# Optimization experiments

Hardware: AMD Instinct MI355X
Metric: run time of the kernel (lower is better)

## Reference

```python
import jax, jax.numpy as jnp
import numpy as np

N = 50000
E = 800000
IN_DIM = 256
HID = 64
HEADS = 4
OUT_DIM = 32
NEG_SLOPE = 0.2
EPS = 1e-5


def segment_softmax(logits, seg, num_segments):
    # logits: [E, H]; softmax over edges sharing the same destination node
    m = jax.ops.segment_max(logits, seg, num_segments=num_segments)
    m = jnp.where(jnp.isfinite(m), m, 0.0)
    e = jnp.exp(logits - m[seg])
    s = jax.ops.segment_sum(e, seg, num_segments=num_segments)
    return e / (s[seg] + 1e-16)


def setup_inputs() -> dict:
    key = jax.random.key(0)
    ks = jax.random.split(key, 16)
    d = {}
    d['x'] = jax.random.normal(ks[0], (N, IN_DIM), dtype=jnp.float32)
    d['edge_index'] = jax.random.randint(ks[1], (2, E), 0, N, dtype=jnp.int64)
    sc = lambda fan: 1.0 / np.sqrt(fan)
    # input transform: Linear(256->128), Linear(128->64)
    d['t1_w'] = jax.random.normal(ks[2], (IN_DIM, IN_DIM // 2), dtype=jnp.float32) * sc(IN_DIM)
    d['t1_b'] = jnp.zeros((IN_DIM // 2,), jnp.float32)
    d['t2_w'] = jax.random.normal(ks[3], (IN_DIM // 2, IN_DIM // 4), dtype=jnp.float32) * sc(IN_DIM // 2)
    d['t2_b'] = jnp.zeros((IN_DIM // 4,), jnp.float32)
    d['g1_w'] = jax.random.normal(ks[4], (IN_DIM // 4, HEADS * HID), dtype=jnp.float32) * sc(IN_DIM // 4)
    d['g1_att_src'] = jax.random.normal(ks[5], (HEADS, HID), dtype=jnp.float32) * sc(HID)
    d['g1_att_dst'] = jax.random.normal(ks[6], (HEADS, HID), dtype=jnp.float32) * sc(HID)
    d['g1_b'] = jnp.zeros((HEADS * HID,), jnp.float32)
    # GraphNorm(256)
    d['gn_w'] = jnp.ones((HEADS * HID,), jnp.float32)
    d['gn_b'] = jnp.zeros((HEADS * HID,), jnp.float32)
    d['gn_ms'] = jnp.ones((HEADS * HID,), jnp.float32)
    # GATConv 2: 256 -> 32, 1 head, no concat (mean == identity for 1 head)
    d['g2_w'] = jax.random.normal(ks[7], (HEADS * HID, OUT_DIM), dtype=jnp.float32) * sc(HEADS * HID)
    d['g2_att_src'] = jax.random.normal(ks[8], (1, OUT_DIM), dtype=jnp.float32) * sc(OUT_DIM)
    d['g2_att_dst'] = jax.random.normal(ks[9], (1, OUT_DIM), dtype=jnp.float32) * sc(OUT_DIM)
    d['g2_b'] = jnp.zeros((OUT_DIM,), jnp.float32)
    return d


def gat_conv(x, src, dst, w, att_src, att_dst, bias, n_nodes):
    heads, ch = att_src.shape
    h = (x @ w).reshape(n_nodes, heads, ch)            # [N,H,C]
    a_src = jnp.sum(h * att_src, axis=-1)              # [N,H]
    a_dst = jnp.sum(h * att_dst, axis=-1)              # [N,H]
    logits = jax.nn.leaky_relu(a_src[src] + a_dst[dst], NEG_SLOPE)  # [E,H]
    alpha = segment_softmax(logits, dst, n_nodes)      # [E,H]
    msgs = alpha[:, :, None] * h[src]                  # [E,H,C]
    out = jax.ops.segment_sum(msgs, dst, num_segments=n_nodes)  # [N,H,C]
    return out.reshape(n_nodes, heads * ch) + bias


def reference(x, edge_index, t1_w, t1_b, t2_w, t2_b,
              g1_w, g1_att_src, g1_att_dst, g1_b,
              gn_w, gn_b, gn_ms,
              g2_w, g2_att_src, g2_att_dst, g2_b):
    src, dst = edge_index[0], edge_index[1]
    # input transform (dropout inactive in eval)
    h = jax.nn.relu(x @ t1_w + t1_b)
    h = jax.nn.relu(h @ t2_w + t2_b)
    # GAT layer 1 (concat heads)
    h = gat_conv(h, src, dst, g1_w, g1_att_src, g1_att_dst, g1_b, N)
    # GraphNorm over the whole graph (batch=None -> single graph)
    mean = jnp.mean(h, axis=0)
    o = h - mean * gn_ms
    var = jnp.mean(o * o, axis=0)
    h = o / jnp.sqrt(var + EPS) * gn_w + gn_b
    h = jax.nn.elu(h)
    # GAT layer 2 (1 head, concat=False)
    h = gat_conv(h, src, dst, g2_w, g2_att_src, g2_att_dst, g2_b, N)
    return jax.nn.log_softmax(h, axis=1)
```

## Files before the change

### kernel.cpp

```cpp
#include <hip/hip_runtime.h>

#define NSLOPE 0.2f
#define GEPS 1e-5f

typedef unsigned short ushortT;
typedef __attribute__((ext_vector_type(8))) unsigned short us8;
typedef __attribute__((ext_vector_type(8))) __bf16 bf16x8;
typedef __attribute__((ext_vector_type(4))) float f32x4;

__device__ __forceinline__ float lrelu(float x) { return x >= 0.f ? x : NSLOPE * x; }
__device__ __forceinline__ ushortT f2bf(float f) {
    unsigned int u = __float_as_uint(f);
    return (ushortT)((u + 0x7fffu + ((u >> 16) & 1u)) >> 16);
}
__device__ __forceinline__ float bf2f(ushortT h) {
    return __uint_as_float((unsigned int)h << 16);
}

__global__ __launch_bounds__(256) void k_prep(
    const float* __restrict__ w1, const float* __restrict__ w2,
    const float* __restrict__ g1w, const float* __restrict__ g2w,
    ushortT* __restrict__ w1t, ushortT* __restrict__ w2t,
    ushortT* __restrict__ g1t, ushortT* __restrict__ g2t)
{
    const int i = blockIdx.x * 256 + threadIdx.x;
    if (i < 128 * 256) { const int c = i >> 8, k = i & 255; w1t[i] = f2bf(w1[k * 128 + c]); }
    if (i < 64 * 128)  { const int c = i >> 7, k = i & 127; w2t[i] = f2bf(w2[k * 64 + c]); }
    if (i < 256 * 64)  { const int c = i >> 6, k = i & 63;  g1t[i] = f2bf(g1w[k * 256 + c]); }
    if (i < 32 * 256)  { const int c = i >> 8, k = i & 255; g2t[i] = f2bf(g2w[k * 32 + c]); }
}

__global__ __launch_bounds__(256) void k_lin1(const float* __restrict__ x,
    const ushortT* __restrict__ w1t, const float* __restrict__ b1,
    ushortT* __restrict__ h1, int n)
{
    __shared__ us8 Ab[64 * 128 / 16];
    __shared__ us8 Bb[128 * 128 / 16];
    char* A = (char*)Ab; char* B = (char*)Bb;
    const int t = threadIdx.x;
    const int w = t >> 6, l = t & 63;
    const int lo = l & 15, hi = l >> 4;
    const int n0 = blockIdx.x * 64;
    const int wm = (w >> 1) * 32, wn = (w & 1) * 64;
    f32x4 acc[2][4];
    #pragma unroll
    for (int mf = 0; mf < 2; ++mf)
        #pragma unroll
        for (int nf = 0; nf < 4; ++nf) acc[mf][nf] = (f32x4){0.f, 0.f, 0.f, 0.f};

    const int arow = t >> 2, ak0 = (t & 3) * 16;
    int agn = n0 + arow; if (agn >= n) agn = n - 1;
    const int asw = (arow & 7) << 4;

    for (int kc = 0; kc < 4; ++kc) {
        __syncthreads();
        {
            ushortT tmp[16];
            const float* xp = &x[(size_t)agn * 256 + kc * 64 + ak0];
            #pragma unroll
            for (int j = 0; j < 4; ++j) {
                const float4 v = *(const float4*)(xp + j * 4);
                tmp[j*4+0] = f2bf(v.x); tmp[j*4+1] = f2bf(v.y);
                tmp[j*4+2] = f2bf(v.z); tmp[j*4+3] = f2bf(v.w);
            }
            *(us8*)(A + arow * 128 + ((ak0 * 2) ^ asw)) = *(us8*)tmp;
            *(us8*)(A + arow * 128 + ((ak0 * 2 + 16) ^ asw)) = *(us8*)(tmp + 8);
        }
        #pragma unroll
        for (int i = 0; i < 4; ++i) {
            const int idx = i * 256 + t, br = idx >> 3, bs = idx & 7;
            const us8 v = *(const us8*)&w1t[(size_t)br * 256 + kc * 64 + bs * 8];
            *(us8*)(B + br * 128 + ((bs * 16) ^ ((br & 7) << 4))) = v;
        }
        __syncthreads();
        #pragma unroll
        for (int ks = 0; ks < 2; ++ks) {
            const int koff = ks * 64 + hi * 16;
            bf16x8 af[2], bf[4];
            #pragma unroll
            for (int mf = 0; mf < 2; ++mf) {
                const int r = wm + mf * 16 + lo;
                af[mf] = *(const bf16x8*)(A + r * 128 + (koff ^ ((r & 7) << 4)));
            }
            #pragma unroll
            for (int nf = 0; nf < 4; ++nf) {
                const int r = wn + nf * 16 + lo;
                bf[nf] = *(const bf16x8*)(B + r * 128 + (koff ^ ((r & 7) << 4)));
            }
            #pragma unroll
            for (int mf = 0; mf < 2; ++mf)
                #pragma unroll
                for (int nf = 0; nf < 4; ++nf)
                    acc[mf][nf] = __builtin_amdgcn_mfma_f32_16x16x32_bf16(af[mf], bf[nf], acc[mf][nf], 0, 0, 0);
        }
    }
    #pragma unroll
    for (int nf = 0; nf < 4; ++nf) {
        const int col = wn + nf * 16 + lo;
        const float bb = b1[col];
        #pragma unroll
        for (int mf = 0; mf < 2; ++mf)
            #pragma unroll
            for (int j = 0; j < 4; ++j) {
                const int r = n0 + wm + mf * 16 + hi * 4 + j;
                if (r < n) h1[(size_t)r * 128 + col] = f2bf(fmaxf(acc[mf][nf][j] + bb, 0.f));
            }
    }
}

__global__ __launch_bounds__(256) void k_lin2(const ushortT* __restrict__ h1,
    const ushortT* __restrict__ w2t, const float* __restrict__ b2,
    ushortT* __restrict__ h2, int n)
{
    __shared__ us8 Ab[64 * 128 / 16];
    __shared__ us8 Bb[64 * 128 / 16];
    char* A = (char*)Ab; char* B = (char*)Bb;
    const int t = threadIdx.x;
    const int w = t >> 6, l = t & 63;
    const int lo = l & 15, hi = l >> 4;
    const int n0 = blockIdx.x * 64;
    const int wm = (w >> 1) * 32, wn = (w & 1) * 32;
    f32x4 acc[2][2];
    #pragma unroll
    for (int mf = 0; mf < 2; ++mf)
        #pragma unroll
        for (int nf = 0; nf < 2; ++nf) acc[mf][nf] = (f32x4){0.f, 0.f, 0.f, 0.f};

    const int arow = t >> 2, ak0 = (t & 3) * 16;
    int agn = n0 + arow; if (agn >= n) agn = n - 1;
    const int asw = (arow & 7) << 4;

    for (int kc = 0; kc < 2; ++kc) {
        __syncthreads();
        {
            const us8 v0 = *(const us8*)&h1[(size_t)agn * 128 + kc * 64 + ak0];
            const us8 v1 = *(const us8*)&h1[(size_t)agn * 128 + kc * 64 + ak0 + 8];
            *(us8*)(A + arow * 128 + ((ak0 * 2) ^ asw)) = v0;
            *(us8*)(A + arow * 128 + ((ak0 * 2 + 16) ^ asw)) = v1;
        }
        #pragma unroll
        for (int i = 0; i < 2; ++i) {
            const int idx = i * 256 + t, br = idx >> 3, bs = idx & 7;
            const us8 v = *(const us8*)&w2t[(size_t)br * 128 + kc * 64 + bs * 8];
            *(us8*)(B + br * 128 + ((bs * 16) ^ ((br & 7) << 4))) = v;
        }
        __syncthreads();
        #pragma unroll
        for (int ks = 0; ks < 2; ++ks) {
            const int koff = ks * 64 + hi * 16;
            bf16x8 af[2], bf[2];
            #pragma unroll
            for (int mf = 0; mf < 2; ++mf) {
                const int r = wm + mf * 16 + lo;
                af[mf] = *(const bf16x8*)(A + r * 128 + (koff ^ ((r & 7) << 4)));
            }
            #pragma unroll
            for (int nf = 0; nf < 2; ++nf) {
                const int r = wn + nf * 16 + lo;
                bf[nf] = *(const bf16x8*)(B + r * 128 + (koff ^ ((r & 7) << 4)));
            }
            #pragma unroll
            for (int mf = 0; mf < 2; ++mf)
                #pragma unroll
                for (int nf = 0; nf < 2; ++nf)
                    acc[mf][nf] = __builtin_amdgcn_mfma_f32_16x16x32_bf16(af[mf], bf[nf], acc[mf][nf], 0, 0, 0);
        }
    }
    #pragma unroll
    for (int nf = 0; nf < 2; ++nf) {
        const int col = wn + nf * 16 + lo;
        const float bb = b2[col];
        #pragma unroll
        for (int mf = 0; mf < 2; ++mf)
            #pragma unroll
            for (int j = 0; j < 4; ++j) {
                const int r = n0 + wm + mf * 16 + hi * 4 + j;
                if (r < n) h2[(size_t)r * 64 + col] = f2bf(fmaxf(acc[mf][nf][j] + bb, 0.f));
            }
    }
}

__global__ __launch_bounds__(256) void k_g1feat(const ushortT* __restrict__ h2,
    const ushortT* __restrict__ g1t, const float* __restrict__ attS, const float* __restrict__ attD,
    ushortT* __restrict__ hg1, float* __restrict__ a1s, float* __restrict__ a1d, int n)
{
    __shared__ us8 Ab[64 * 128 / 16];
    __shared__ us8 Bb[256 * 128 / 16];
    char* A = (char*)Ab; char* B = (char*)Bb;
    const int t = threadIdx.x;
    const int w = t >> 6, l = t & 63;
    const int lo = l & 15, hi = l >> 4;
    const int n0 = blockIdx.x * 64;
    const int wm = (w >> 1) * 32, wn = (w & 1) * 128;
    f32x4 acc[2][8];
    #pragma unroll
    for (int mf = 0; mf < 2; ++mf)
        #pragma unroll
        for (int nf = 0; nf < 8; ++nf) acc[mf][nf] = (f32x4){0.f, 0.f, 0.f, 0.f};

    {
        const int arow = t >> 2, ak0 = (t & 3) * 16;
        int agn = n0 + arow; if (agn >= n) agn = n - 1;
        const int asw = (arow & 7) << 4;
        const us8 v0 = *(const us8*)&h2[(size_t)agn * 64 + ak0];
        const us8 v1 = *(const us8*)&h2[(size_t)agn * 64 + ak0 + 8];
        *(us8*)(A + arow * 128 + ((ak0 * 2) ^ asw)) = v0;
        *(us8*)(A + arow * 128 + ((ak0 * 2 + 16) ^ asw)) = v1;
    }
    #pragma unroll
    for (int i = 0; i < 8; ++i) {
        const int idx = i * 256 + t, br = idx >> 3, bs = idx & 7;
        const us8 v = *(const us8*)&g1t[(size_t)br * 64 + bs * 8];
        *(us8*)(B + br * 128 + ((bs * 16) ^ ((br & 7) << 4))) = v;
    }
    __syncthreads();
    #pragma unroll
    for (int ks = 0; ks < 2; ++ks) {
        const int koff = ks * 64 + hi * 16;
        bf16x8 af[2];
        #pragma unroll
        for (int mf = 0; mf < 2; ++mf) {
            const int r = wm + mf * 16 + lo;
            af[mf] = *(const bf16x8*)(A + r * 128 + (koff ^ ((r & 7) << 4)));
        }
        #pragma unroll
        for (int nf = 0; nf < 8; ++nf) {
            const int r = wn + nf * 16 + lo;
            const bf16x8 bf = *(const bf16x8*)(B + r * 128 + (koff ^ ((r & 7) << 4)));
            #pragma unroll
            for (int mf = 0; mf < 2; ++mf)
                acc[mf][nf] = __builtin_amdgcn_mfma_f32_16x16x32_bf16(af[mf], bf, acc[mf][nf], 0, 0, 0);
        }
    }
    float sS[8], sD[8];
    #pragma unroll
    for (int nf = 0; nf < 8; ++nf) {
        sS[nf] = attS[wn + nf * 16 + lo];
        sD[nf] = attD[wn + nf * 16 + lo];
    }
    const int hA = wn >> 6, hB = hA + 1;
    #pragma unroll
    for (int mf = 0; mf < 2; ++mf)
        #pragma unroll
        for (int j = 0; j < 4; ++j) {
            const int r = n0 + wm + mf * 16 + hi * 4 + j;
            float pSA = 0.f, pDA = 0.f, pSB = 0.f, pDB = 0.f;
            #pragma unroll
            for (int nf = 0; nf < 4; ++nf) {
                pSA = fmaf(acc[mf][nf][j], sS[nf], pSA);
                pDA = fmaf(acc[mf][nf][j], sD[nf], pDA);
                pSB = fmaf(acc[mf][nf + 4][j], sS[nf + 4], pSB);
                pDB = fmaf(acc[mf][nf + 4][j], sD[nf + 4], pDB);
            }
            #pragma unroll
            for (int off = 1; off < 16; off <<= 1) {
                pSA += __shfl_xor(pSA, off);
                pDA += __shfl_xor(pDA, off);
                pSB += __shfl_xor(pSB, off);
                pDB += __shfl_xor(pDB, off);
            }
            if (r < n) {
                if (lo == 0) {
                    a1s[r * 4 + hA] = pSA; a1s[r * 4 + hB] = pSB;
                    a1d[r * 4 + hA] = pDA; a1d[r * 4 + hB] = pDB;
                }
                #pragma unroll
                for (int nf = 0; nf < 8; ++nf)
                    hg1[(size_t)r * 256 + wn + nf * 16 + lo] = f2bf(acc[mf][nf][j]);
            }
        }
}

__global__ __launch_bounds__(256) void k_g2feat(const ushortT* __restrict__ out1,
    const float* __restrict__ cscale, const float* __restrict__ cshift,
    const ushortT* __restrict__ g2t, const float* __restrict__ attS, const float* __restrict__ attD,
    ushortT* __restrict__ hg2, float* __restrict__ a2s, float* __restrict__ a2d, int n)
{
    __shared__ us8 Ab[64 * 128 / 16];
    __shared__ us8 Bb[32 * 128 / 16];
    char* A = (char*)Ab; char* B = (char*)Bb;
    const int t = threadIdx.x;
    const int w = t >> 6, l = t & 63;
    const int lo = l & 15, hi = l >> 4;
    const int n0 = blockIdx.x * 64;
    const int wm = w * 16;
    f32x4 acc[2];
    acc[0] = (f32x4){0.f, 0.f, 0.f, 0.f};
    acc[1] = (f32x4){0.f, 0.f, 0.f, 0.f};

    const int arow = t >> 2, ak0 = (t & 3) * 16;
    int agn = n0 + arow; if (agn >= n) agn = n - 1;
    const int asw = (arow & 7) << 4;

    for (int kc = 0; kc < 4; ++kc) {
        __syncthreads();
        {
            ushortT tmp[16];
            const us8 v0 = *(const us8*)&out1[(size_t)agn * 256 + kc * 64 + ak0];
            const us8 v1 = *(const us8*)&out1[(size_t)agn * 256 + kc * 64 + ak0 + 8];
            #pragma unroll
            for (int j = 0; j < 8; ++j) {
                float a = bf2f(v0[j]) * cscale[kc * 64 + ak0 + j] + cshift[kc * 64 + ak0 + j];
                float b = bf2f(v1[j]) * cscale[kc * 64 + ak0 + 8 + j] + cshift[kc * 64 + ak0 + 8 + j];
                a = a > 0.f ? a : __expf(a) - 1.f;
                b = b > 0.f ? b : __expf(b) - 1.f;
                tmp[j] = f2bf(a); tmp[8 + j] = f2bf(b);
            }
            *(us8*)(A + arow * 128 + ((ak0 * 2) ^ asw)) = *(us8*)tmp;
            *(us8*)(A + arow * 128 + ((ak0 * 2 + 16) ^ asw)) = *(us8*)(tmp + 8);
        }
        {
            const int br = t >> 3, bs = t & 7;
            const us8 v = *(const us8*)&g2t[(size_t)br * 256 + kc * 64 + bs * 8];
            *(us8*)(B + br * 128 + ((bs * 16) ^ ((br & 7) << 4))) = v;
        }
        __syncthreads();
        #pragma unroll
        for (int ks = 0; ks < 2; ++ks) {
            const int koff = ks * 64 + hi * 16;
            const int ra = wm + lo;
            const bf16x8 af = *(const bf16x8*)(A + ra * 128 + (koff ^ ((ra & 7) << 4)));
            #pragma unroll
            for (int nf = 0; nf < 2; ++nf) {
                const int r = nf * 16 + lo;
                const bf16x8 bf = *(const bf16x8*)(B + r * 128 + (koff ^ ((r & 7) << 4)));
                acc[nf] = __builtin_amdgcn_mfma_f32_16x16x32_bf16(af, bf, acc[nf], 0, 0, 0);
            }
        }
    }
    float sS[2], sD[2];
    sS[0] = attS[lo]; sS[1] = attS[16 + lo];
    sD[0] = attD[lo]; sD[1] = attD[16 + lo];
    #pragma unroll
    for (int j = 0; j < 4; ++j) {
        const int r = n0 + wm + hi * 4 + j;
        float pS = fmaf(acc[0][j], sS[0], acc[1][j] * sS[1]);
        float pD = fmaf(acc[0][j], sD[0], acc[1][j] * sD[1]);
        #pragma unroll
        for (int off = 1; off < 16; off <<= 1) {
            pS += __shfl_xor(pS, off);
            pD += __shfl_xor(pD, off);
        }
        if (r < n) {
            if (lo == 0) { a2s[r] = pS; a2d[r] = pD; }
            hg2[(size_t)r * 32 + lo] = f2bf(acc[0][j]);
            hg2[(size_t)r * 32 + 16 + lo] = f2bf(acc[1][j]);
        }
    }
}

__global__ void k_hist(const int* __restrict__ dst, int* __restrict__ deg, int e) {
    int i = blockIdx.x * 256 + threadIdx.x;
    if (i < e) atomicAdd(&deg[dst[i]], 1);
}

__global__ __launch_bounds__(256) void k_scan1(const int* __restrict__ deg, int* __restrict__ offs,
                                               int* __restrict__ bsum, int n)
{
    __shared__ int sm[256];
    const int t = threadIdx.x;
    const int i = blockIdx.x * 256 + t;
    const int v = (i < n) ? deg[i] : 0;
    sm[t] = v;
    __syncthreads();
    for (int off = 1; off < 256; off <<= 1) {
        int add = (t >= off) ? sm[t - off] : 0;
        __syncthreads();
        sm[t] += add;
        __syncthreads();
    }
    if (i < n) offs[i] = sm[t] - v;
    if (t == 255) bsum[blockIdx.x] = sm[255];
}

__global__ __launch_bounds__(256) void k_scan2(int* __restrict__ bsum, int nb) {
    __shared__ int sm[256];
    const int t = threadIdx.x;
    const int v = (t < nb) ? bsum[t] : 0;
    sm[t] = v;
    __syncthreads();
    for (int off = 1; off < 256; off <<= 1) {
        int add = (t >= off) ? sm[t - off] : 0;
        __syncthreads();
        sm[t] += add;
        __syncthreads();
    }
    if (t < nb) bsum[t] = sm[t] - v;
}

__global__ void k_scan3(int* __restrict__ offs, int* __restrict__ cursor,
                        const int* __restrict__ bsum, int n, int e) {
    int i = blockIdx.x * 256 + threadIdx.x;
    if (i < n) {
        int o = offs[i] + bsum[i >> 8];
        offs[i] = o;
        cursor[i] = o;
    }
    if (i == 0) offs[n] = e;
}

__global__ void k_scatter(const int* __restrict__ src, const int* __restrict__ dst,
                          int* __restrict__ cursor, int* __restrict__ csr, int e) {
    int i = blockIdx.x * 256 + threadIdx.x;
    if (i < e) {
        int p = atomicAdd(&cursor[dst[i]], 1);
        csr[p] = src[i];
    }
}

__global__ __launch_bounds__(256) void k_alpha1(
    const float* __restrict__ a1s, const float* __restrict__ a1d,
    const int* __restrict__ offs, const int* __restrict__ csr,
    float* __restrict__ alphaE, int n)
{
    const int l = threadIdx.x & 15;
    const int d = blockIdx.x * 16 + (threadIdx.x >> 4);
    if (d >= n) return;
    const int start = offs[d], end = offs[d + 1];
    const float4* __restrict__ a1s4 = (const float4*)a1s;
    const float4 adv = ((const float4*)a1d)[d];
    const float ad0 = adv.x, ad1 = adv.y, ad2 = adv.z, ad3 = adv.w;

    float m0 = -1e30f, m1 = -1e30f, m2 = -1e30f, m3 = -1e30f;
    float s0 = 0.f, s1 = 0.f, s2 = 0.f, s3 = 0.f;
    for (int e = start + l; e < end; e += 16) {
        const float4 av = a1s4[csr[e]];
        const float l0 = lrelu(av.x + ad0), l1 = lrelu(av.y + ad1);
        const float l2 = lrelu(av.z + ad2), l3 = lrelu(av.w + ad3);
        float nm;
        nm = fmaxf(m0, l0); s0 = s0 * __expf(m0 - nm) + __expf(l0 - nm); m0 = nm;
        nm = fmaxf(m1, l1); s1 = s1 * __expf(m1 - nm) + __expf(l1 - nm); m1 = nm;
        nm = fmaxf(m2, l2); s2 = s2 * __expf(m2 - nm) + __expf(l2 - nm); m2 = nm;
        nm = fmaxf(m3, l3); s3 = s3 * __expf(m3 - nm) + __expf(l3 - nm); m3 = nm;
    }
    for (int off = 1; off < 16; off <<= 1) {
        float om, os, nm;
        om = __shfl_xor(m0, off, 16); os = __shfl_xor(s0, off, 16);
        nm = fmaxf(m0, om); s0 = s0 * __expf(m0 - nm) + os * __expf(om - nm); m0 = nm;
        om = __shfl_xor(m1, off, 16); os = __shfl_xor(s1, off, 16);
        nm = fmaxf(m1, om); s1 = s1 * __expf(m1 - nm) + os * __expf(om - nm); m1 = nm;
        om = __shfl_xor(m2, off, 16); os = __shfl_xor(s2, off, 16);
        nm = fmaxf(m2, om); s2 = s2 * __expf(m2 - nm) + os * __expf(om - nm); m2 = nm;
        om = __shfl_xor(m3, off, 16); os = __shfl_xor(s3, off, 16);
        nm = fmaxf(m3, om); s3 = s3 * __expf(m3 - nm) + os * __expf(om - nm); m3 = nm;
    }
    const float i0 = 1.f / (s0 + 1e-16f), i1 = 1.f / (s1 + 1e-16f);
    const float i2 = 1.f / (s2 + 1e-16f), i3 = 1.f / (s3 + 1e-16f);
    for (int e = start + l; e < end; e += 16) {
        const float4 av = a1s4[csr[e]];
        float4 o;
        o.x = __expf(lrelu(av.x + ad0) - m0) * i0;
        o.y = __expf(lrelu(av.y + ad1) - m1) * i1;
        o.z = __expf(lrelu(av.z + ad2) - m2) * i2;
        o.w = __expf(lrelu(av.w + ad3) - m3) * i3;
        *(float4*)&alphaE[(size_t)e * 4] = o;
    }
}

__global__ __launch_bounds__(256, 8) void k_pv1(
    const ushortT* __restrict__ hg1, const float* __restrict__ alphaE,
    const int* __restrict__ offs, const int* __restrict__ csr,
    const float* __restrict__ bias, ushortT* __restrict__ out1, int n)
{
    const int lane = threadIdx.x & 63;
    const int d = blockIdx.x * 4 + (threadIdx.x >> 6);
    if (d >= n) return;
    const int start = offs[d], end = offs[d + 1];
    const int cg = lane & 31;
    const int c = cg * 8;
    const int es = lane >> 5;
    const int head = cg >> 3;
    float acc[8];
    #pragma unroll
    for (int j = 0; j < 8; ++j) acc[j] = 0.f;

    #pragma unroll 4
    for (int e = start + es; e < end; e += 2) {
        const int si = csr[e];
        const float al = alphaE[(size_t)e * 4 + head];
        const us8 hv = *(const us8*)&hg1[(size_t)si * 256 + c];
        #pragma unroll
        for (int j = 0; j < 8; ++j) acc[j] = fmaf(al, bf2f(hv[j]), acc[j]);
    }
    #pragma unroll
    for (int j = 0; j < 8; ++j) acc[j] += __shfl_xor(acc[j], 32);
    if (es == 0) {
        const float4 b0 = *(const float4*)&bias[c];
        const float4 b1 = *(const float4*)&bias[c + 4];
        us8 o;
        o[0] = f2bf(acc[0] + b0.x); o[1] = f2bf(acc[1] + b0.y);
        o[2] = f2bf(acc[2] + b0.z); o[3] = f2bf(acc[3] + b0.w);
        o[4] = f2bf(acc[4] + b1.x); o[5] = f2bf(acc[5] + b1.y);
        o[6] = f2bf(acc[6] + b1.z); o[7] = f2bf(acc[7] + b1.w);
        *(us8*)&out1[(size_t)d * 256 + c] = o;
    }
}

__global__ __launch_bounds__(256) void k_colstat(const ushortT* __restrict__ out1,
    float* __restrict__ colsum, float* __restrict__ colsq, int n)
{
    const int t = threadIdx.x;
    float s = 0.f, q = 0.f;
    for (int r = blockIdx.x; r < n; r += gridDim.x) {
        const float v = bf2f(out1[(size_t)r * 256 + t]);
        s += v;
        q += v * v;
    }
    atomicAdd(&colsum[t], s);
    atomicAdd(&colsq[t], q);
}

__global__ void k_norm_params(const float* __restrict__ colsum, const float* __restrict__ colsq,
    const float* __restrict__ gw, const float* __restrict__ gb, const float* __restrict__ gms,
    float* __restrict__ scale, float* __restrict__ shift, int n)
{
    const int t = threadIdx.x;
    const float invn = 1.f / (float)n;
    const float mean = colsum[t] * invn;
    const float msq = colsq[t] * invn;
    const float ms = gms[t];
    const float var = msq - 2.f * ms * mean * mean + ms * ms * mean * mean;
    const float sc = gw[t] * rsqrtf(var + GEPS);
    scale[t] = sc;
    shift[t] = gb[t] - mean * ms * sc;
}

__global__ __launch_bounds__(256) void k_alpha2(
    const float* __restrict__ a2s, const float* __restrict__ a2d,
    const int* __restrict__ offs, const int* __restrict__ csr,
    float* __restrict__ alphaE2, int n)
{
    const int l = threadIdx.x & 15;
    const int d = blockIdx.x * 16 + (threadIdx.x >> 4);
    if (d >= n) return;
    const int start = offs[d], end = offs[d + 1];
    const float adv = a2d[d];
    float m = -1e30f, s = 0.f;
    for (int e = start + l; e < end; e += 16) {
        const float lv = lrelu(a2s[csr[e]] + adv);
        const float nm = fmaxf(m, lv);
        s = s * __expf(m - nm) + __expf(lv - nm);
        m = nm;
    }
    for (int off = 1; off < 16; off <<= 1) {
        const float om = __shfl_xor(m, off, 16), os = __shfl_xor(s, off, 16);
        const float nm = fmaxf(m, om);
        s = s * __expf(m - nm) + os * __expf(om - nm);
        m = nm;
    }
    const float inv = 1.f / (s + 1e-16f);
    for (int e = start + l; e < end; e += 16)
        alphaE2[e] = __expf(lrelu(a2s[csr[e]] + adv) - m) * inv;
}

__global__ __launch_bounds__(256, 8) void k_pv2(
    const ushortT* __restrict__ hg2, const float* __restrict__ alphaE2,
    const int* __restrict__ offs, const int* __restrict__ csr,
    const float* __restrict__ bias, float* __restrict__ out, int n)
{
    const int l = threadIdx.x & 15;
    const int d = blockIdx.x * 16 + (threadIdx.x >> 4);
    if (d >= n) return;
    const int start = offs[d], end = offs[d + 1];
    const int c = l * 2;
    float acc0 = 0.f, acc1 = 0.f;
    #pragma unroll 8
    for (int e = start; e < end; ++e) {
        const int si = csr[e];
        const float al = alphaE2[e];
        const ushort2 hv = *(const ushort2*)&hg2[(size_t)si * 32 + c];
        acc0 = fmaf(al, bf2f(hv.x), acc0);
        acc1 = fmaf(al, bf2f(hv.y), acc1);
    }
    const float v0 = acc0 + bias[c];
    const float v1 = acc1 + bias[c + 1];
    float mx = fmaxf(v0, v1);
    for (int off = 1; off < 16; off <<= 1) mx = fmaxf(mx, __shfl_xor(mx, off, 16));
    float se = __expf(v0 - mx) + __expf(v1 - mx);
    for (int off = 1; off < 16; off <<= 1) se += __shfl_xor(se, off, 16);
    const float ls = __logf(se);
    float2 o = {v0 - mx - ls, v1 - mx - ls};
    *(float2*)&out[(size_t)d * 32 + c] = o;
}

extern "C" void kernel_launch(void* const* d_in, const int* in_sizes, int n_in,
                              void* d_out, int out_size, void* d_ws, size_t ws_size,
                              hipStream_t stream)
{
    const float* x    = (const float*)d_in[0];
    const int*   ei   = (const int*)d_in[1];
    const float* t1w  = (const float*)d_in[2];
    const float* t1b  = (const float*)d_in[3];
    const float* t2w  = (const float*)d_in[4];
    const float* t2b  = (const float*)d_in[5];
    const float* g1w  = (const float*)d_in[6];
    const float* g1as = (const float*)d_in[7];
    const float* g1ad = (const float*)d_in[8];
    const float* g1b  = (const float*)d_in[9];
    const float* gnw  = (const float*)d_in[10];
    const float* gnb  = (const float*)d_in[11];
    const float* gnms = (const float*)d_in[12];
    const float* g2w  = (const float*)d_in[13];
    const float* g2as = (const float*)d_in[14];
    const float* g2ad = (const float*)d_in[15];
    const float* g2b  = (const float*)d_in[16];

    const int N = in_sizes[0] / 256;
    const int E = in_sizes[1] / 2;
    const int* srcA = ei;
    const int* dstA = ei + E;

    char* ws = (char*)d_ws;
    size_t cur = 0;
    auto alloc = [&](size_t bytes) -> char* {
        char* p = ws + cur;
        cur += (bytes + 255) & ~(size_t)255;
        return p;
    };
    ushortT* h1      = (ushortT*)alloc((size_t)N * 128 * 2);
    ushortT* h2      = (ushortT*)alloc((size_t)N * 64 * 2);
    ushortT* hg1     = (ushortT*)alloc((size_t)N * 256 * 2);
    float*   a1s     = (float*)alloc((size_t)N * 4 * 4);
    float*   a1d     = (float*)alloc((size_t)N * 4 * 4);
    ushortT* out1    = (ushortT*)alloc((size_t)N * 256 * 2);
    ushortT* hg2     = (ushortT*)alloc((size_t)N * 32 * 2);
    float*   a2s     = (float*)alloc((size_t)N * 4);
    float*   a2d     = (float*)alloc((size_t)N * 4);
    int*     deg     = (int*)alloc((size_t)(N + 1) * 4);
    int*     offs    = (int*)alloc((size_t)(N + 1) * 4);
    int*     cursor  = (int*)alloc((size_t)N * 4);
    int*     bsum    = (int*)alloc(1024);
    int*     csr     = (int*)alloc((size_t)E * 4);
    float*   alphaE  = (float*)alloc((size_t)E * 4 * 4);
    float*   alphaE2 = (float*)alloc((size_t)E * 4);
    float*   colsum  = (float*)alloc(1024);
    float*   colsq   = (float*)alloc(1024);
    float*   cscale  = (float*)alloc(1024);
    float*   cshift  = (float*)alloc(1024);
    ushortT* w1t     = (ushortT*)alloc(128 * 256 * 2);
    ushortT* w2t     = (ushortT*)alloc(64 * 128 * 2);
    ushortT* g1t     = (ushortT*)alloc(256 * 64 * 2);
    ushortT* g2t     = (ushortT*)alloc(32 * 256 * 2);

    hipMemsetAsync(deg, 0, (size_t)(N + 1) * 4, stream);
    hipMemsetAsync(colsum, 0, 2048, stream);

    const int EB  = (E + 255) / 256;
    const int NB  = (N + 255) / 256;
    const int B64 = (N + 63) / 64;
    const int B16 = (N + 15) / 16;
    const int B4  = (N + 3) / 4;

    k_prep<<<128, 256, 0, stream>>>(t1w, t2w, g1w, g2w, w1t, w2t, g1t, g2t);
    k_lin1<<<B64, 256, 0, stream>>>(x, w1t, t1b, h1, N);
    k_lin2<<<B64, 256, 0, stream>>>(h1, w2t, t2b, h2, N);
    k_g1feat<<<B64, 256, 0, stream>>>(h2, g1t, g1as, g1ad, hg1, a1s, a1d, N);
    k_hist<<<EB, 256, 0, stream>>>(dstA, deg, E);
    k_scan1<<<NB, 256, 0, stream>>>(deg, offs, bsum, N);
    k_scan2<<<1, 256, 0, stream>>>(bsum, NB);
    k_scan3<<<NB, 256, 0, stream>>>(offs, cursor, bsum, N, E);
    k_scatter<<<EB, 256, 0, stream>>>(srcA, dstA, cursor, csr, E);
    k_alpha1<<<B16, 256, 0, stream>>>(a1s, a1d, offs, csr, alphaE, N);
    k_pv1<<<B4, 256, 0, stream>>>(hg1, alphaE, offs, csr, g1b, out1, N);
    k_colstat<<<256, 256, 0, stream>>>(out1, colsum, colsq, N);
    k_norm_params<<<1, 256, 0, stream>>>(colsum, colsq, gnw, gnb, gnms, cscale, cshift, N);
    k_g2feat<<<B64, 256, 0, stream>>>(out1, cscale, cshift, g2t, g2as, g2ad, hg2, a2s, a2d, N);
    k_alpha2<<<B16, 256, 0, stream>>>(a2s, a2d, offs, csr, alphaE2, N);
    k_pv2<<<B16, 256, 0, stream>>>(hg2, alphaE2, offs, csr, g2b, (float*)d_out, N);
}
```

Measured before the change: 320.5 us.

## Fold CSR build into GEMM launches, store attention weights in fp16, split pv2 edges

The histogram, the three scan stages and the offset fixup are merged into the weight-prep and GEMM kernels as extra blocks, which removes four kernel launches and lets the small CSR work run alongside the GEMMs. Per-edge attention coefficients are stored as fp16 instead of fp32, halving their write and read traffic in both GAT layers at some precision cost. The second aggregation kernel now gives each node 32 lanes that split its edges into two interleaved streams and combine them with a shuffle. The extra branch in each GEMM kernel adds shared-memory pressure and divergence, and the fp16 coefficients may introduce small numerical error.

```diff
diff --git a/kernel.cpp b/kernel.cpp
--- a/kernel.cpp
+++ b/kernel.cpp
@@ -16,13 +16,25 @@
 __device__ __forceinline__ float bf2f(ushortT h) {
     return __uint_as_float((unsigned int)h << 16);
 }
-
-__global__ __launch_bounds__(256) void k_prep(
+__device__ __forceinline__ ushortT f2h(float f) {
+    union { _Float16 h; ushortT u; } v; v.h = (_Float16)f; return v.u;
+}
+__device__ __forceinline__ float h2f(ushortT u) {
+    union { _Float16 h; ushortT u; } v; v.u = u; return (float)v.h;
+}
+
+__global__ __launch_bounds__(256) void k_prep_hist(
     const float* __restrict__ w1, const float* __restrict__ w2,
     const float* __restrict__ g1w, const float* __restrict__ g2w,
     ushortT* __restrict__ w1t, ushortT* __restrict__ w2t,
-    ushortT* __restrict__ g1t, ushortT* __restrict__ g2t)
-{
+    ushortT* __restrict__ g1t, ushortT* __restrict__ g2t,
+    const int* __restrict__ dst, int* __restrict__ deg, int E)
+{
+    if (blockIdx.x >= 128) {
+        const int i = (blockIdx.x - 128) * 256 + threadIdx.x;
+        if (i < E) atomicAdd(&deg[dst[i]], 1);
+        return;
+    }
     const int i = blockIdx.x * 256 + threadIdx.x;
     if (i < 128 * 256) { const int c = i >> 8, k = i & 255; w1t[i] = f2bf(w1[k * 128 + c]); }
     if (i < 64 * 128)  { const int c = i >> 7, k = i & 127; w2t[i] = f2bf(w2[k * 64 + c]); }
@@ -32,8 +44,26 @@
 
 __global__ __launch_bounds__(256) void k_lin1(const float* __restrict__ x,
     const ushortT* __restrict__ w1t, const float* __restrict__ b1,
-    ushortT* __restrict__ h1, int n)
-{
+    ushortT* __restrict__ h1, int n,
+    const int* __restrict__ deg, int* __restrict__ offs, int* __restrict__ bsum, int gemmB)
+{
+    if ((int)blockIdx.x >= gemmB) {
+        __shared__ int sm[256];
+        const int t = threadIdx.x;
+        const int i = (blockIdx.x - gemmB) * 256 + t;
+        const int v = (i < n) ? deg[i] : 0;
+        sm[t] = v;
+        __syncthreads();
+        for (int off = 1; off < 256; off <<= 1) {
+            int add = (t >= off) ? sm[t - off] : 0;
+            __syncthreads();
+            sm[t] += add;
+            __syncthreads();
+        }
+        if (i < n) offs[i] = sm[t] - v;
+        if (t == 255) bsum[blockIdx.x - gemmB] = sm[255];
+        return;
+    }
     __shared__ us8 Ab[64 * 128 / 16];
     __shared__ us8 Bb[128 * 128 / 16];
     char* A = (char*)Ab; char* B = (char*)Bb;
@@ -110,8 +140,24 @@
 
 __global__ __launch_bounds__(256) void k_lin2(const ushortT* __restrict__ h1,
     const ushortT* __restrict__ w2t, const float* __restrict__ b2,
-    ushortT* __restrict__ h2, int n)
-{
+    ushortT* __restrict__ h2, int n,
+    int* __restrict__ bsum, int nb, int gemmB)
+{
+    if ((int)blockIdx.x >= gemmB) {
+        __shared__ int sm[256];
+        const int t = threadIdx.x;
+        const int v = (t < nb) ? bsum[t] : 0;
+        sm[t] = v;
+        __syncthreads();
+        for (int off = 1; off < 256; off <<= 1) {
+            int add = (t >= off) ? sm[t - off] : 0;
+            __syncthreads();
+            sm[t] += add;
+            __syncthreads();
+        }
+        if (t < nb) bsum[t] = sm[t] - v;
+        return;
+    }
     __shared__ us8 Ab[64 * 128 / 16];
     __shared__ us8 Bb[64 * 128 / 16];
     char* A = (char*)Ab; char* B = (char*)Bb;
@@ -182,8 +228,20 @@
 
 __global__ __launch_bounds__(256) void k_g1feat(const ushortT* __restrict__ h2,
     const ushortT* __restrict__ g1t, const float* __restrict__ attS, const float* __restrict__ attD,
-    ushortT* __restrict__ hg1, float* __restrict__ a1s, float* __restrict__ a1d, int n)
-{
+    ushortT* __restrict__ hg1, float* __restrict__ a1s, float* __restrict__ a1d, int n,
+    int* __restrict__ offs, int* __restrict__ cursor, const int* __restrict__ bsum, int E, int gemmB)
+{
+    if ((int)blockIdx.x >= gemmB) {
+        const int sb = blockIdx.x - gemmB;
+        const int i = sb * 256 + threadIdx.x;
+        if (i < n) {
+            int o = offs[i] + bsum[i >> 8];
+            offs[i] = o;
+            cursor[i] = o;
+        }
+        if (i == 0) offs[n] = E;
+        return;
+    }
     __shared__ us8 Ab[64 * 128 / 16];
     __shared__ us8 Bb[256 * 128 / 16];
     char* A = (char*)Ab; char* B = (char*)Bb;
@@ -349,56 +407,6 @@
     }
 }
 
-__global__ void k_hist(const int* __restrict__ dst, int* __restrict__ deg, int e) {
-    int i = blockIdx.x * 256 + threadIdx.x;
-    if (i < e) atomicAdd(&deg[dst[i]], 1);
-}
-
-__global__ __launch_bounds__(256) void k_scan1(const int* __restrict__ deg, int* __restrict__ offs,
-                                               int* __restrict__ bsum, int n)
-{
-    __shared__ int sm[256];
-    const int t = threadIdx.x;
-    const int i = blockIdx.x * 256 + t;
-    const int v = (i < n) ? deg[i] : 0;
-    sm[t] = v;
-    __syncthreads();
-    for (int off = 1; off < 256; off <<= 1) {
-        int add = (t >= off) ? sm[t - off] : 0;
-        __syncthreads();
-        sm[t] += add;
-        __syncthreads();
-    }
-    if (i < n) offs[i] = sm[t] - v;
-    if (t == 255) bsum[blockIdx.x] = sm[255];
-}
-
-__global__ __launch_bounds__(256) void k_scan2(int* __restrict__ bsum, int nb) {
-    __shared__ int sm[256];
-    const int t = threadIdx.x;
-    const int v = (t < nb) ? bsum[t] : 0;
-    sm[t] = v;
-    __syncthreads();
-    for (int off = 1; off < 256; off <<= 1) {
-        int add = (t >= off) ? sm[t - off] : 0;
-        __syncthreads();
-        sm[t] += add;
-        __syncthreads();
-    }
-    if (t < nb) bsum[t] = sm[t] - v;
-}
-
-__global__ void k_scan3(int* __restrict__ offs, int* __restrict__ cursor,
-                        const int* __restrict__ bsum, int n, int e) {
-    int i = blockIdx.x * 256 + threadIdx.x;
-    if (i < n) {
-        int o = offs[i] + bsum[i >> 8];
-        offs[i] = o;
-        cursor[i] = o;
-    }
-    if (i == 0) offs[n] = e;
-}
-
 __global__ void k_scatter(const int* __restrict__ src, const int* __restrict__ dst,
                           int* __restrict__ cursor, int* __restrict__ csr, int e) {
     int i = blockIdx.x * 256 + threadIdx.x;
@@ -411,7 +419,7 @@
 __global__ __launch_bounds__(256) void k_alpha1(
     const float* __restrict__ a1s, const float* __restrict__ a1d,
     const int* __restrict__ offs, const int* __restrict__ csr,
-    float* __restrict__ alphaE, int n)
+    ushortT* __restrict__ alphaH, int n)
 {
     const int l = threadIdx.x & 15;
     const int d = blockIdx.x * 16 + (threadIdx.x >> 4);
@@ -448,17 +456,17 @@
     const float i2 = 1.f / (s2 + 1e-16f), i3 = 1.f / (s3 + 1e-16f);
     for (int e = start + l; e < end; e += 16) {
         const float4 av = a1s4[csr[e]];
-        float4 o;
-        o.x = __expf(lrelu(av.x + ad0) - m0) * i0;
-        o.y = __expf(lrelu(av.y + ad1) - m1) * i1;
-        o.z = __expf(lrelu(av.z + ad2) - m2) * i2;
-        o.w = __expf(lrelu(av.w + ad3) - m3) * i3;
-        *(float4*)&alphaE[(size_t)e * 4] = o;
+        ushort4 o;
+        o.x = f2h(__expf(lrelu(av.x + ad0) - m0) * i0);
+        o.y = f2h(__expf(lrelu(av.y + ad1) - m1) * i1);
+        o.z = f2h(__expf(lrelu(av.z + ad2) - m2) * i2);
+        o.w = f2h(__expf(lrelu(av.w + ad3) - m3) * i3);
+        *(ushort4*)&alphaH[(size_t)e * 4] = o;
     }
 }
 
 __global__ __launch_bounds__(256, 8) void k_pv1(
-    const ushortT* __restrict__ hg1, const float* __restrict__ alphaE,
+    const ushortT* __restrict__ hg1, const ushortT* __restrict__ alphaH,
     const int* __restrict__ offs, const int* __restrict__ csr,
     const float* __restrict__ bias, ushortT* __restrict__ out1, int n)
 {
@@ -477,7 +485,7 @@
     #pragma unroll 4
     for (int e = start + es; e < end; e += 2) {
         const int si = csr[e];
-        const float al = alphaE[(size_t)e * 4 + head];
+        const float al = h2f(alphaH[(size_t)e * 4 + head]);
         const us8 hv = *(const us8*)&hg1[(size_t)si * 256 + c];
         #pragma unroll
         for (int j = 0; j < 8; ++j) acc[j] = fmaf(al, bf2f(hv[j]), acc[j]);
@@ -528,7 +536,7 @@
 __global__ __launch_bounds__(256) void k_alpha2(
     const float* __restrict__ a2s, const float* __restrict__ a2d,
     const int* __restrict__ offs, const int* __restrict__ csr,
-    float* __restrict__ alphaE2, int n)
+    ushortT* __restrict__ alphaH2, int n)
 {
     const int l = threadIdx.x & 15;
     const int d = blockIdx.x * 16 + (threadIdx.x >> 4);
@@ -550,28 +558,31 @@
     }
     const float inv = 1.f / (s + 1e-16f);
     for (int e = start + l; e < end; e += 16)
-        alphaE2[e] = __expf(lrelu(a2s[csr[e]] + adv) - m) * inv;
+        alphaH2[e] = f2h(__expf(lrelu(a2s[csr[e]] + adv) - m) * inv);
 }
 
 __global__ __launch_bounds__(256, 8) void k_pv2(
-    const ushortT* __restrict__ hg2, const float* __restrict__ alphaE2,
+    const ushortT* __restrict__ hg2, const ushortT* __restrict__ alphaH2,
     const int* __restrict__ offs, const int* __restrict__ csr,
     const float* __restrict__ bias, float* __restrict__ out, int n)
 {
-    const int l = threadIdx.x & 15;
-    const int d = blockIdx.x * 16 + (threadIdx.x >> 4);
+    const int lane = threadIdx.x & 31;
+    const int d = blockIdx.x * 8 + (threadIdx.x >> 5);
     if (d >= n) return;
     const int start = offs[d], end = offs[d + 1];
+    const int l = lane & 15, es = lane >> 4;
     const int c = l * 2;
     float acc0 = 0.f, acc1 = 0.f;
-    #pragma unroll 8
-    for (int e = start; e < end; ++e) {
+    #pragma unroll 4
+    for (int e = start + es; e < end; e += 2) {
         const int si = csr[e];
-        const float al = alphaE2[e];
+        const float al = h2f(alphaH2[e]);
         const ushort2 hv = *(const ushort2*)&hg2[(size_t)si * 32 + c];
         acc0 = fmaf(al, bf2f(hv.x), acc0);
         acc1 = fmaf(al, bf2f(hv.y), acc1);
     }
+    acc0 += __shfl_xor(acc0, 16, 32);
+    acc1 += __shfl_xor(acc1, 16, 32);
     const float v0 = acc0 + bias[c];
     const float v1 = acc1 + bias[c + 1];
     float mx = fmaxf(v0, v1);
@@ -579,8 +590,10 @@
     float se = __expf(v0 - mx) + __expf(v1 - mx);
     for (int off = 1; off < 16; off <<= 1) se += __shfl_xor(se, off, 16);
     const float ls = __logf(se);
-    float2 o = {v0 - mx - ls, v1 - mx - ls};
-    *(float2*)&out[(size_t)d * 32 + c] = o;
+    if (es == 0) {
+        float2 o = {v0 - mx - ls, v1 - mx - ls};
+        *(float2*)&out[(size_t)d * 32 + c] = o;
+    }
 }
 
 extern "C" void kernel_launch(void* const* d_in, const int* in_sizes, int n_in,
@@ -631,8 +644,8 @@
     int*     cursor  = (int*)alloc((size_t)N * 4);
     int*     bsum    = (int*)alloc(1024);
     int*     csr     = (int*)alloc((size_t)E * 4);
-    float*   alphaE  = (float*)alloc((size_t)E * 4 * 4);
-    float*   alphaE2 = (float*)alloc((size_t)E * 4);
+    ushortT* alphaH  = (ushortT*)alloc((size_t)E * 4 * 2);
+    ushortT* alphaH2 = (ushortT*)alloc((size_t)E * 2);
     float*   colsum  = (float*)alloc(1024);
     float*   colsq   = (float*)alloc(1024);
     float*   cscale  = (float*)alloc(1024);
@@ -649,22 +662,19 @@
     const int NB  = (N + 255) / 256;
     const int B64 = (N + 63) / 64;
     const int B16 = (N + 15) / 16;
+    const int B8  = (N + 7) / 8;
     const int B4  = (N + 3) / 4;
 
-    k_prep<<<128, 256, 0, stream>>>(t1w, t2w, g1w, g2w, w1t, w2t, g1t, g2t);
-    k_lin1<<<B64, 256, 0, stream>>>(x, w1t, t1b, h1, N);
-    k_lin2<<<B64, 256, 0, stream>>>(h1, w2t, t2b, h2, N);
-    k_g1feat<<<B64, 256, 0, stream>>>(h2, g1t, g1as, g1ad, hg1, a1s, a1d, N);
-    k_hist<<<EB, 256, 0, stream>>>(dstA, deg, E);
-    k_scan1<<<NB, 256, 0, stream>>>(deg, offs, bsum, N);
-    k_scan2<<<1, 256, 0, stream>>>(bsum, NB);
-    k_scan3<<<NB, 256, 0, stream>>>(offs, cursor, bsum, N, E);
+    k_prep_hist<<<128 + EB, 256, 0, stream>>>(t1w, t2w, g1w, g2w, w1t, w2t, g1t, g2t, dstA, deg, E);
+    k_lin1<<<B64 + NB, 256, 0, stream>>>(x, w1t, t1b, h1, N, deg, offs, bsum, B64);
+    k_lin2<<<B64 + 1, 256, 0, stream>>>(h1, w2t, t2b, h2, N, bsum, NB, B64);
+    k_g1feat<<<B64 + NB, 256, 0, stream>>>(h2, g1t, g1as, g1ad, hg1, a1s, a1d, N, offs, cursor, bsum, E, B64);
     k_scatter<<<EB, 256, 0, stream>>>(srcA, dstA, cursor, csr, E);
-    k_alpha1<<<B16, 256, 0, stream>>>(a1s, a1d, offs, csr, alphaE, N);
-    k_pv1<<<B4, 256, 0, stream>>>(hg1, alphaE, offs, csr, g1b, out1, N);
+    k_alpha1<<<B16, 256, 0, stream>>>(a1s, a1d, offs, csr, alphaH, N);
+    k_pv1<<<B4, 256, 0, stream>>>(hg1, alphaH, offs, csr, g1b, out1, N);
     k_colstat<<<256, 256, 0, stream>>>(out1, colsum, colsq, N);
     k_norm_params<<<1, 256, 0, stream>>>(colsum, colsq, gnw, gnb, gnms, cscale, cshift, N);
     k_g2feat<<<B64, 256, 0, stream>>>(out1, cscale, cshift, g2t, g2as, g2ad, hg2, a2s, a2d, N);
-    k_alpha2<<<B16, 256, 0, stream>>>(a2s, a2d, offs, csr, alphaE2, N);
-    k_pv2<<<B16, 256, 0, stream>>>(hg2, alphaE2, offs, csr, g2b, (float*)d_out, N);
-}
+    k_alpha2<<<B16, 256, 0, stream>>>(a2s, a2d, offs, csr, alphaH2, N);
+    k_pv2<<<B8, 256, 0, stream>>>(hg2, alphaH2, offs, csr, g2b, (float*)d_out, N);
+}
```

Result: faster. 305.7 us (-4.6%).
